# Performance work log

Measured on AMD Instinct MI355X. Metric: run time of the kernel, lower is better.

## Reference

```python
import jax, jax.numpy as jnp
import numpy as np

H = 16   # multiheads
DH = 64  # head_dim


def setup_inputs() -> dict:
    key = jax.random.key(0)
    ks = jax.random.split(key, 9)
    B, S, D = 4, 2048, H * DH
    scale = 1.0 / np.sqrt(D)
    return {
        "Q_seq": jax.random.normal(ks[0], (B, S, D), dtype=jnp.float32),
        "K_seq": jax.random.normal(ks[1], (B, S, D), dtype=jnp.float32),
        "V_seq": jax.random.normal(ks[2], (B, S, D), dtype=jnp.float32),
        "WQ_w": jax.random.normal(ks[3], (D, D), dtype=jnp.float32) * scale,
        "WQ_b": jax.random.normal(ks[4], (D,), dtype=jnp.float32) * 0.02,
        "WK_w": jax.random.normal(ks[5], (D, D), dtype=jnp.float32) * scale,
        "WK_b": jax.random.normal(ks[6], (D,), dtype=jnp.float32) * 0.02,
        "WV_w": jax.random.normal(ks[7], (D, D), dtype=jnp.float32) * scale,
        "WV_b": jax.random.normal(ks[8], (D,), dtype=jnp.float32) * 0.02,
    }


def reference(Q_seq, K_seq, V_seq, WQ_w, WQ_b, WK_w, WK_b, WV_w, WV_b):
    B, Sq, D = Q_seq.shape
    Sk = K_seq.shape[1]
    # torch nn.Linear: y = x @ W.T + b
    Q = (Q_seq @ WQ_w.T + WQ_b).reshape(B, Sq, H, DH).transpose(0, 2, 1, 3)  # bhqd
    K = (K_seq @ WK_w.T + WK_b).reshape(B, Sk, H, DH).transpose(0, 2, 1, 3)  # bhkd
    V = (V_seq @ WV_w.T + WV_b).reshape(B, Sk, H, DH).transpose(0, 2, 1, 3)  # bhkd
    inv_sqrt_d = jnp.float32(1.0 / np.sqrt(DH))
    A = jnp.einsum('bhqd,bhkd->bhqk', Q, K) * inv_sqrt_d
    A = jax.nn.softmax(A, axis=-1)
    O = jnp.einsum('bhqk,bhkd->bhqd', A, V)
    return O.transpose(0, 2, 1, 3).reshape(B, Sq, H * DH)
```

## Files before the change

### kernel.cpp

```cpp
#include <hip/hip_runtime.h>

#define HH 16
#define DHH 64
#define BB 4
#define SS 2048
#define DD 1024

typedef __attribute__((ext_vector_type(8))) short short8;
typedef __attribute__((ext_vector_type(4))) float f32x4;
typedef __attribute__((ext_vector_type(16))) float f32x16;

__device__ __forceinline__ unsigned short f2bf(float f) {
  union { float f; unsigned int u; } v; v.f = f;
  unsigned int r = v.u + 0x7fffu + ((v.u >> 16) & 1u);
  return (unsigned short)(r >> 16);
}
__device__ __forceinline__ unsigned cvt_pk_bf16(float a, float b) {
  unsigned r;
  asm("v_cvt_pk_bf16_f32 %0, %1, %2" : "=v"(r) : "v"(a), "v"(b));
  return r;
}

__global__ __launch_bounds__(256) void proj_kernel(
    const float* __restrict__ X, const float* __restrict__ W,
    const float* __restrict__ bias, unsigned short* __restrict__ out,
    int mode, float scale)
{
  __shared__ unsigned short As[128 * 40];
  __shared__ unsigned short Bs[128 * 40];

  const int t    = threadIdx.x;
  const int pb   = blockIdx.x;
  const int lb   = (pb & 7) * 64 + (pb >> 3);
  const int m0   = (lb >> 3) * 128;
  const int n0   = (lb & 7) * 128;
  const int rowA = t >> 3;
  const int kc   = (t & 7) * 4;
  const int lane = t & 63;
  const int wid  = t >> 6;
  const int wm   = (wid >> 1) * 64;
  const int wn   = (wid & 1) * 64;
  const int g    = lane >> 4;
  const int c    = lane & 15;

  f32x4 acc[4][4];
#pragma unroll
  for (int i = 0; i < 4; ++i)
#pragma unroll
    for (int j = 0; j < 4; ++j) acc[i][j] = (f32x4){0.f, 0.f, 0.f, 0.f};

  float4 xa[4], wb[4];
#pragma unroll
  for (int p4 = 0; p4 < 4; ++p4) {
    const int r = p4 * 32 + rowA;
    xa[p4] = *reinterpret_cast<const float4*>(X + (size_t)(m0 + r) * DD + kc);
    wb[p4] = *reinterpret_cast<const float4*>(W + (size_t)(n0 + r) * DD + kc);
  }

  for (int kt = 0; kt < 32; ++kt) {
    __syncthreads();
#pragma unroll
    for (int p4 = 0; p4 < 4; ++p4) {
      const int r = p4 * 32 + rowA;
      unsigned* da = reinterpret_cast<unsigned*>(&As[r * 40 + kc]);
      unsigned* db = reinterpret_cast<unsigned*>(&Bs[r * 40 + kc]);
      da[0] = cvt_pk_bf16(xa[p4].x, xa[p4].y);
      da[1] = cvt_pk_bf16(xa[p4].z, xa[p4].w);
      db[0] = cvt_pk_bf16(wb[p4].x, wb[p4].y);
      db[1] = cvt_pk_bf16(wb[p4].z, wb[p4].w);
    }
    __syncthreads();
    if (kt < 31) {
#pragma unroll
      for (int p4 = 0; p4 < 4; ++p4) {
        const int r = p4 * 32 + rowA;
        xa[p4] = *reinterpret_cast<const float4*>(
            X + (size_t)(m0 + r) * DD + (kt + 1) * 32 + kc);
        wb[p4] = *reinterpret_cast<const float4*>(
            W + (size_t)(n0 + r) * DD + (kt + 1) * 32 + kc);
      }
    }
    short8 a[4], b[4];
#pragma unroll
    for (int mf = 0; mf < 4; ++mf)
      a[mf] = *reinterpret_cast<const short8*>(&As[(wm + mf * 16 + c) * 40 + g * 8]);
#pragma unroll
    for (int nf = 0; nf < 4; ++nf)
      b[nf] = *reinterpret_cast<const short8*>(&Bs[(wn + nf * 16 + c) * 40 + g * 8]);
#pragma unroll
    for (int mf = 0; mf < 4; ++mf)
#pragma unroll
      for (int nf = 0; nf < 4; ++nf)
        acc[mf][nf] = __builtin_amdgcn_mfma_f32_16x16x32_bf16(
            a[mf], b[nf], acc[mf][nf], 0, 0, 0);
  }

#pragma unroll
  for (int nf = 0; nf < 4; ++nf) {
    const int col  = n0 + wn + nf * 16 + c;
    const float bv = bias[col];
    const int hcol = col >> 6;
    const int dcol = col & 63;
#pragma unroll
    for (int mf = 0; mf < 4; ++mf) {
      const int row0 = m0 + wm + mf * 16 + g * 4;
      const int bi   = row0 >> 11;
      const int s0   = row0 & 2047;
      if (mode < 2) {
        const size_t base = ((size_t)(bi * HH + hcol) * SS + s0) * DHH + dcol;
#pragma unroll
        for (int r = 0; r < 4; ++r)
          out[base + (size_t)r * DHH] = f2bf((acc[mf][nf][r] + bv) * scale);
      } else {
        const size_t base = ((size_t)(bi * HH + hcol) * DHH + dcol) * SS + s0;
        unsigned* dp = reinterpret_cast<unsigned*>(out + base);
        dp[0] = cvt_pk_bf16(acc[mf][nf][0] + bv, acc[mf][nf][1] + bv);
        dp[1] = cvt_pk_bf16(acc[mf][nf][2] + bv, acc[mf][nf][3] + bv);
      }
    }
  }
}

__global__ __launch_bounds__(256, 4) void attn_kernel(
    const unsigned short* __restrict__ Qb,
    const unsigned short* __restrict__ Kb,
    const unsigned short* __restrict__ Vt,
    float* __restrict__ O)
{
  __shared__ unsigned short sm[16384];

  const int t    = threadIdx.x;
  const int lane = t & 63;
  const int w    = t >> 6;
  const int h    = lane >> 5;
  const int c5   = lane & 31;
  const int cx   = c5 & 7;

  const int p  = blockIdx.x;
  const int l  = (p & 7) * 128 + (p >> 3);
  const int bh = l >> 4;
  const int qb = l & 15;
  const int q0 = qb * 128 + w * 32;

  const unsigned short* Qp = Qb + (size_t)bh * SS * DHH;
  const unsigned short* Kp = Kb + (size_t)bh * SS * DHH;
  const unsigned short* Vp = Vt + (size_t)bh * DHH * SS;

  const int srow   = t >> 3;
  const int schunk = (t & 7) ^ (srow & 7);

  auto STAGE = [&](int buf, int kt) {
    const int kk0 = kt * 64;
#pragma unroll
    for (int j = 0; j < 2; ++j) {
      const unsigned short* gk = Kp + (size_t)(kk0 + j * 32 + srow) * DHH + schunk * 8;
      const unsigned short* gv = Vp + (size_t)(j * 32 + srow) * SS + kk0 + schunk * 8;
      __builtin_amdgcn_global_load_lds(
          (const __attribute__((address_space(1))) void*)gk,
          (__attribute__((address_space(3))) void*)(sm + buf * 8192 + j * 2048 + w * 512),
          16, 0, 0);
      __builtin_amdgcn_global_load_lds(
          (const __attribute__((address_space(1))) void*)gv,
          (__attribute__((address_space(3))) void*)(sm + buf * 8192 + 4096 + j * 2048 + w * 512),
          16, 0, 0);
    }
  };

  short8 bq[4];
#pragma unroll
  for (int k4 = 0; k4 < 4; ++k4)
    bq[k4] = *reinterpret_cast<const short8*>(
        Qp + (size_t)(q0 + c5) * DHH + k4 * 16 + h * 8);

  STAGE(0, 0);

  f32x16 oa0, oa1;
#pragma unroll
  for (int i = 0; i < 16; ++i) { oa0[i] = 0.f; oa1[i] = 0.f; }
  float m_run = -1e30f, l_part = 0.f;

  __syncthreads();

  for (int kt = 0; kt < SS / 64; ++kt) {
    const int buf = kt & 1;
    if (kt + 1 < SS / 64) STAGE(buf ^ 1, kt + 1);

    const unsigned short* Kl = sm + buf * 8192;
    const unsigned short* Vl = Kl + 4096;

    f32x16 st0, st1;
#pragma unroll
    for (int i = 0; i < 16; ++i) { st0[i] = 0.f; st1[i] = 0.f; }
#pragma unroll
    for (int k4 = 0; k4 < 4; ++k4) {
      const int pos = ((2 * k4 + h) ^ cx) * 8;
      short8 ak0 = *reinterpret_cast<const short8*>(Kl + c5 * 64 + pos);
      short8 ak1 = *reinterpret_cast<const short8*>(Kl + (32 + c5) * 64 + pos);
      st0 = __builtin_amdgcn_mfma_f32_32x32x16_bf16(ak0, bq[k4], st0, 0, 0, 0);
      st1 = __builtin_amdgcn_mfma_f32_32x32x16_bf16(ak1, bq[k4], st1, 0, 0, 0);
    }

    float mloc = st0[0];
#pragma unroll
    for (int i = 1; i < 16; ++i) mloc = fmaxf(mloc, st0[i]);
#pragma unroll
    for (int i = 0; i < 16; ++i) mloc = fmaxf(mloc, st1[i]);
    mloc = fmaxf(mloc, __shfl_xor(mloc, 32));

    if (!__all(mloc <= m_run + 11.0f)) {
      const float mn = fmaxf(m_run, mloc);
      const float al = exp2f(m_run - mn);
      l_part *= al;
#pragma unroll
      for (int i = 0; i < 16; ++i) { oa0[i] *= al; oa1[i] *= al; }
      m_run = mn;
    }

#pragma unroll
    for (int i = 0; i < 16; ++i) { st0[i] = exp2f(st0[i] - m_run); l_part += st0[i]; }
#pragma unroll
    for (int i = 0; i < 16; ++i) { st1[i] = exp2f(st1[i] - m_run); l_part += st1[i]; }

    unsigned pw[16];
#pragma unroll
    for (int m4 = 0; m4 < 4; ++m4)
#pragma unroll
      for (int t2 = 0; t2 < 2; ++t2) {
        pw[m4 * 2 + t2]     = cvt_pk_bf16(st0[m4 * 4 + 2 * t2], st0[m4 * 4 + 2 * t2 + 1]);
        pw[8 + m4 * 2 + t2] = cvt_pk_bf16(st1[m4 * 4 + 2 * t2], st1[m4 * 4 + 2 * t2 + 1]);
      }

#pragma unroll
    for (int ks = 0; ks < 4; ++ks) {
      union { unsigned u[4]; short8 s8; } pbu;
#pragma unroll
      for (int t2 = 0; t2 < 2; ++t2) {
        const unsigned e  = pw[4 * ks + t2];
        const unsigned o  = pw[4 * ks + 2 + t2];
        const unsigned ce = (unsigned)__shfl_xor((int)e, 32);
        const unsigned co = (unsigned)__shfl_xor((int)o, 32);
        pbu.u[t2]     = h ? co : e;
        pbu.u[2 + t2] = h ? o  : ce;
      }
      const int vpos = ((2 * ks + h) ^ cx) * 8;
      short8 av0 = *reinterpret_cast<const short8*>(Vl + c5 * 64 + vpos);
      short8 av1 = *reinterpret_cast<const short8*>(Vl + (32 + c5) * 64 + vpos);
      oa0 = __builtin_amdgcn_mfma_f32_32x32x16_bf16(av0, pbu.s8, oa0, 0, 0, 0);
      oa1 = __builtin_amdgcn_mfma_f32_32x32x16_bf16(av1, pbu.s8, oa1, 0, 0, 0);
    }
    __syncthreads();
  }

  const float lt  = l_part + __shfl_xor(l_part, 32);
  const float inv = 1.f / lt;
  const int b = bh >> 4, hd = bh & 15;
  float* Orow = O + ((size_t)(b * SS) + q0 + c5) * DD + hd * DHH;
#pragma unroll
  for (int m4 = 0; m4 < 4; ++m4) {
    f32x4 v0, v1;
#pragma unroll
    for (int r = 0; r < 4; ++r) {
      v0[r] = oa0[m4 * 4 + r] * inv;
      v1[r] = oa1[m4 * 4 + r] * inv;
    }
    *reinterpret_cast<f32x4*>(Orow + m4 * 8 + 4 * h)      = v0;
    *reinterpret_cast<f32x4*>(Orow + 32 + m4 * 8 + 4 * h) = v1;
  }
}

extern "C" void kernel_launch(void* const* d_in, const int* in_sizes, int n_in,
                              void* d_out, int out_size, void* d_ws, size_t ws_size,
                              hipStream_t stream) {
  (void)in_sizes; (void)n_in; (void)out_size; (void)ws_size;
  const float* Xq = (const float*)d_in[0];
  const float* Xk = (const float*)d_in[1];
  const float* Xv = (const float*)d_in[2];
  const float* WQ = (const float*)d_in[3];
  const float* bQ = (const float*)d_in[4];
  const float* WK = (const float*)d_in[5];
  const float* bK = (const float*)d_in[6];
  const float* WV = (const float*)d_in[7];
  const float* bV = (const float*)d_in[8];
  float* O = (float*)d_out;

  const size_t elems = (size_t)BB * HH * SS * DHH;
  unsigned short* Qbuf = (unsigned short*)d_ws;
  unsigned short* Kbuf = Qbuf + elems;
  unsigned short* Vbuf = Kbuf + elems;

  const float CLOG = 0.125f * 1.4426950408889634f;
  proj_kernel<<<512, 256, 0, stream>>>(Xq, WQ, bQ, Qbuf, 0, CLOG);
  proj_kernel<<<512, 256, 0, stream>>>(Xk, WK, bK, Kbuf, 1, 1.0f);
  proj_kernel<<<512, 256, 0, stream>>>(Xv, WV, bV, Vbuf, 2, 1.0f);

  attn_kernel<<<1024, 256, 0, stream>>>(Qbuf, Kbuf, Vbuf, O);
}
```

Before: 380.3 us.

## Pre-convert inputs to bf16 and restructure projection and attention inner loops

Adds a separate fp32-to-bf16 conversion pass so the projection GEMM can stream bf16 tiles into swizzled, double-buffered LDS with global_load_lds, using a larger K step. The attention kernel folds the running max into the accumulator init, uses max3 reductions, raw v_exp_f32, permlane32 swaps instead of shuffles, and s_setprio around MFMA blocks. This removes in-loop conversion and register staging from the GEMM and trims VALU work in softmax, at the cost of extra kernel launches and a full read/write pass over the activations and weights.

```diff
diff --git a/kernel.cpp b/kernel.cpp
--- a/kernel.cpp
+++ b/kernel.cpp
@@ -5,6 +5,8 @@
 #define BB 4
 #define SS 2048
 #define DD 1024
+#define XN 8388608
+#define WN 1048576
 
 typedef __attribute__((ext_vector_type(8))) short short8;
 typedef __attribute__((ext_vector_type(4))) float f32x4;
@@ -20,28 +22,75 @@
   asm("v_cvt_pk_bf16_f32 %0, %1, %2" : "=v"(r) : "v"(a), "v"(b));
   return r;
 }
+__device__ __forceinline__ float fast_exp2(float x) {
+  float r;
+  asm("v_exp_f32 %0, %1" : "=v"(r) : "v"(x));
+  return r;
+}
+__device__ __forceinline__ float m3(float a, float b, float c) {
+  float r;
+  asm("v_max3_f32 %0, %1, %2, %3" : "=v"(r) : "v"(a), "v"(b), "v"(c));
+  return r;
+}
+__device__ __forceinline__ void plswap(unsigned& a, unsigned& b) {
+  auto r = __builtin_amdgcn_permlane32_swap(a, b, false, false);
+  a = r[0]; b = r[1];
+}
+
+__global__ __launch_bounds__(256) void conv_kernel(
+    const float* __restrict__ X, const float* __restrict__ W,
+    unsigned short* __restrict__ Xb, unsigned short* __restrict__ Wb)
+{
+  const size_t gid = (size_t)blockIdx.x * 256 + threadIdx.x;
+  const float* src; unsigned short* dst; size_t off;
+  if (gid < XN / 8) { src = X; dst = Xb; off = gid * 8; }
+  else              { src = W; dst = Wb; off = (gid - XN / 8) * 8; }
+  const float4 a = *reinterpret_cast<const float4*>(src + off);
+  const float4 b = *reinterpret_cast<const float4*>(src + off + 4);
+  unsigned r[4] = { cvt_pk_bf16(a.x, a.y), cvt_pk_bf16(a.z, a.w),
+                    cvt_pk_bf16(b.x, b.y), cvt_pk_bf16(b.z, b.w) };
+  *reinterpret_cast<uint4*>(dst + off) = *reinterpret_cast<uint4*>(r);
+}
 
 __global__ __launch_bounds__(256) void proj_kernel(
-    const float* __restrict__ X, const float* __restrict__ W,
+    const unsigned short* __restrict__ Xb, const unsigned short* __restrict__ Wb,
     const float* __restrict__ bias, unsigned short* __restrict__ out,
     int mode, float scale)
 {
-  __shared__ unsigned short As[128 * 40];
-  __shared__ unsigned short Bs[128 * 40];
+  __shared__ unsigned short As[2][128 * 64];
+  __shared__ unsigned short Bs[2][128 * 64];
 
   const int t    = threadIdx.x;
   const int pb   = blockIdx.x;
   const int lb   = (pb & 7) * 64 + (pb >> 3);
   const int m0   = (lb >> 3) * 128;
   const int n0   = (lb & 7) * 128;
-  const int rowA = t >> 3;
-  const int kc   = (t & 7) * 4;
   const int lane = t & 63;
   const int wid  = t >> 6;
   const int wm   = (wid >> 1) * 64;
   const int wn   = (wid & 1) * 64;
   const int g    = lane >> 4;
   const int c    = lane & 15;
+  const int cx   = c & 7;
+
+  const int srow = t >> 3;
+  const int sch  = (t & 7) ^ (srow & 7);
+
+  auto STAGE = [&](int buf, int k0) {
+#pragma unroll
+    for (int i = 0; i < 4; ++i) {
+      const unsigned short* ga = Xb + (size_t)(m0 + i * 32 + srow) * DD + k0 + sch * 8;
+      const unsigned short* gb = Wb + (size_t)(n0 + i * 32 + srow) * DD + k0 + sch * 8;
+      __builtin_amdgcn_global_load_lds(
+          (const __attribute__((address_space(1))) void*)ga,
+          (__attribute__((address_space(3))) void*)(&As[buf][0] + i * 2048 + wid * 512),
+          16, 0, 0);
+      __builtin_amdgcn_global_load_lds(
+          (const __attribute__((address_space(1))) void*)gb,
+          (__attribute__((address_space(3))) void*)(&Bs[buf][0] + i * 2048 + wid * 512),
+          16, 0, 0);
+    }
+  };
 
   f32x4 acc[4][4];
 #pragma unroll
@@ -49,50 +98,38 @@
 #pragma unroll
     for (int j = 0; j < 4; ++j) acc[i][j] = (f32x4){0.f, 0.f, 0.f, 0.f};
 
-  float4 xa[4], wb[4];
-#pragma unroll
-  for (int p4 = 0; p4 < 4; ++p4) {
-    const int r = p4 * 32 + rowA;
-    xa[p4] = *reinterpret_cast<const float4*>(X + (size_t)(m0 + r) * DD + kc);
-    wb[p4] = *reinterpret_cast<const float4*>(W + (size_t)(n0 + r) * DD + kc);
-  }
-
-  for (int kt = 0; kt < 32; ++kt) {
+  STAGE(0, 0);
+
+  for (int kt = 0; kt < 16; ++kt) {
+    const int buf = kt & 1;
     __syncthreads();
-#pragma unroll
-    for (int p4 = 0; p4 < 4; ++p4) {
-      const int r = p4 * 32 + rowA;
-      unsigned* da = reinterpret_cast<unsigned*>(&As[r * 40 + kc]);
-      unsigned* db = reinterpret_cast<unsigned*>(&Bs[r * 40 + kc]);
-      da[0] = cvt_pk_bf16(xa[p4].x, xa[p4].y);
-      da[1] = cvt_pk_bf16(xa[p4].z, xa[p4].w);
-      db[0] = cvt_pk_bf16(wb[p4].x, wb[p4].y);
-      db[1] = cvt_pk_bf16(wb[p4].z, wb[p4].w);
-    }
-    __syncthreads();
-    if (kt < 31) {
-#pragma unroll
-      for (int p4 = 0; p4 < 4; ++p4) {
-        const int r = p4 * 32 + rowA;
-        xa[p4] = *reinterpret_cast<const float4*>(
-            X + (size_t)(m0 + r) * DD + (kt + 1) * 32 + kc);
-        wb[p4] = *reinterpret_cast<const float4*>(
-            W + (size_t)(n0 + r) * DD + (kt + 1) * 32 + kc);
-      }
-    }
-    short8 a[4], b[4];
-#pragma unroll
-    for (int mf = 0; mf < 4; ++mf)
-      a[mf] = *reinterpret_cast<const short8*>(&As[(wm + mf * 16 + c) * 40 + g * 8]);
-#pragma unroll
-    for (int nf = 0; nf < 4; ++nf)
-      b[nf] = *reinterpret_cast<const short8*>(&Bs[(wn + nf * 16 + c) * 40 + g * 8]);
-#pragma unroll
-    for (int mf = 0; mf < 4; ++mf)
-#pragma unroll
-      for (int nf = 0; nf < 4; ++nf)
-        acc[mf][nf] = __builtin_amdgcn_mfma_f32_16x16x32_bf16(
-            a[mf], b[nf], acc[mf][nf], 0, 0, 0);
+    if (kt < 15) STAGE(buf ^ 1, (kt + 1) * 64);
+
+    short8 a[4][2], b[4][2];
+#pragma unroll
+    for (int mf = 0; mf < 4; ++mf) {
+      const int row = wm + mf * 16 + c;
+#pragma unroll
+      for (int ks = 0; ks < 2; ++ks)
+        a[mf][ks] = *reinterpret_cast<const short8*>(
+            &As[buf][row * 64 + (((ks * 4 + g) ^ cx)) * 8]);
+    }
+#pragma unroll
+    for (int nf = 0; nf < 4; ++nf) {
+      const int row = wn + nf * 16 + c;
+#pragma unroll
+      for (int ks = 0; ks < 2; ++ks)
+        b[nf][ks] = *reinterpret_cast<const short8*>(
+            &Bs[buf][row * 64 + (((ks * 4 + g) ^ cx)) * 8]);
+    }
+#pragma unroll
+    for (int ks = 0; ks < 2; ++ks)
+#pragma unroll
+      for (int mf = 0; mf < 4; ++mf)
+#pragma unroll
+        for (int nf = 0; nf < 4; ++nf)
+          acc[mf][nf] = __builtin_amdgcn_mfma_f32_16x16x32_bf16(
+              a[mf][ks], b[nf][ks], acc[mf][nf], 0, 0, 0);
   }
 
 #pragma unroll
@@ -177,7 +214,7 @@
   f32x16 oa0, oa1;
 #pragma unroll
   for (int i = 0; i < 16; ++i) { oa0[i] = 0.f; oa1[i] = 0.f; }
-  float m_run = -1e30f, l_part = 0.f;
+  float m_run = 0.f, l_part = 0.f;
 
   __syncthreads();
 
@@ -189,8 +226,11 @@
     const unsigned short* Vl = Kl + 4096;
 
     f32x16 st0, st1;
-#pragma unroll
-    for (int i = 0; i < 16; ++i) { st0[i] = 0.f; st1[i] = 0.f; }
+    const float nm = -m_run;
+#pragma unroll
+    for (int i = 0; i < 16; ++i) { st0[i] = nm; st1[i] = nm; }
+
+    __builtin_amdgcn_s_setprio(1);
 #pragma unroll
     for (int k4 = 0; k4 < 4; ++k4) {
       const int pos = ((2 * k4 + h) ^ cx) * 8;
@@ -199,27 +239,54 @@
       st0 = __builtin_amdgcn_mfma_f32_32x32x16_bf16(ak0, bq[k4], st0, 0, 0, 0);
       st1 = __builtin_amdgcn_mfma_f32_32x32x16_bf16(ak1, bq[k4], st1, 0, 0, 0);
     }
-
-    float mloc = st0[0];
-#pragma unroll
-    for (int i = 1; i < 16; ++i) mloc = fmaxf(mloc, st0[i]);
-#pragma unroll
-    for (int i = 0; i < 16; ++i) mloc = fmaxf(mloc, st1[i]);
-    mloc = fmaxf(mloc, __shfl_xor(mloc, 32));
-
-    if (!__all(mloc <= m_run + 11.0f)) {
-      const float mn = fmaxf(m_run, mloc);
-      const float al = exp2f(m_run - mn);
+    __builtin_amdgcn_s_setprio(0);
+
+    float a0 = m3(st0[0], st0[1], st0[2]);
+    float a1 = m3(st0[3], st0[4], st0[5]);
+    float a2 = m3(st0[6], st0[7], st0[8]);
+    float a3 = m3(st0[9], st0[10], st0[11]);
+    float a4 = m3(st0[12], st0[13], st0[14]);
+    float a5 = m3(st0[15], st1[0], st1[1]);
+    float a6 = m3(st1[2], st1[3], st1[4]);
+    float a7 = m3(st1[5], st1[6], st1[7]);
+    float a8 = m3(st1[8], st1[9], st1[10]);
+    float a9 = m3(st1[11], st1[12], st1[13]);
+    float a10 = fmaxf(st1[14], st1[15]);
+    float b0 = m3(a0, a1, a2);
+    float b1 = m3(a3, a4, a5);
+    float b2 = m3(a6, a7, a8);
+    float b3 = m3(a9, a10, b0);
+    float mloc = m3(b1, b2, b3);
+    {
+      unsigned ua = __float_as_uint(mloc), ub = ua;
+      plswap(ua, ub);
+      mloc = fmaxf(__uint_as_float(ua), __uint_as_float(ub));
+    }
+
+    if (!__all(mloc <= 11.0f)) {
+      const float d  = fmaxf(mloc, 0.f);
+      const float al = exp2f(-d);
       l_part *= al;
 #pragma unroll
       for (int i = 0; i < 16; ++i) { oa0[i] *= al; oa1[i] *= al; }
-      m_run = mn;
-    }
-
-#pragma unroll
-    for (int i = 0; i < 16; ++i) { st0[i] = exp2f(st0[i] - m_run); l_part += st0[i]; }
-#pragma unroll
-    for (int i = 0; i < 16; ++i) { st1[i] = exp2f(st1[i] - m_run); l_part += st1[i]; }
+#pragma unroll
+      for (int i = 0; i < 16; ++i) { st0[i] -= d; st1[i] -= d; }
+      m_run += d;
+    }
+
+    float l0 = 0.f, l1 = 0.f, l2 = 0.f, l3 = 0.f;
+#pragma unroll
+    for (int i = 0; i < 16; i += 4) {
+      st0[i]     = fast_exp2(st0[i]);     l0 += st0[i];
+      st0[i + 1] = fast_exp2(st0[i + 1]); l1 += st0[i + 1];
+      st0[i + 2] = fast_exp2(st0[i + 2]); l2 += st0[i + 2];
+      st0[i + 3] = fast_exp2(st0[i + 3]); l3 += st0[i + 3];
+      st1[i]     = fast_exp2(st1[i]);     l0 += st1[i];
+      st1[i + 1] = fast_exp2(st1[i + 1]); l1 += st1[i + 1];
+      st1[i + 2] = fast_exp2(st1[i + 2]); l2 += st1[i + 2];
+      st1[i + 3] = fast_exp2(st1[i + 3]); l3 += st1[i + 3];
+    }
+    l_part += (l0 + l1) + (l2 + l3);
 
     unsigned pw[16];
 #pragma unroll
@@ -230,17 +297,17 @@
         pw[8 + m4 * 2 + t2] = cvt_pk_bf16(st1[m4 * 4 + 2 * t2], st1[m4 * 4 + 2 * t2 + 1]);
       }
 
+    __builtin_amdgcn_s_setprio(1);
 #pragma unroll
     for (int ks = 0; ks < 4; ++ks) {
       union { unsigned u[4]; short8 s8; } pbu;
 #pragma unroll
       for (int t2 = 0; t2 < 2; ++t2) {
-        const unsigned e  = pw[4 * ks + t2];
-        const unsigned o  = pw[4 * ks + 2 + t2];
-        const unsigned ce = (unsigned)__shfl_xor((int)e, 32);
-        const unsigned co = (unsigned)__shfl_xor((int)o, 32);
-        pbu.u[t2]     = h ? co : e;
-        pbu.u[2 + t2] = h ? o  : ce;
+        unsigned a = pw[4 * ks + t2];
+        unsigned b = pw[4 * ks + 2 + t2];
+        plswap(a, b);
+        pbu.u[t2]     = a;
+        pbu.u[2 + t2] = b;
       }
       const int vpos = ((2 * ks + h) ^ cx) * 8;
       short8 av0 = *reinterpret_cast<const short8*>(Vl + c5 * 64 + vpos);
@@ -248,10 +315,13 @@
       oa0 = __builtin_amdgcn_mfma_f32_32x32x16_bf16(av0, pbu.s8, oa0, 0, 0, 0);
       oa1 = __builtin_amdgcn_mfma_f32_32x32x16_bf16(av1, pbu.s8, oa1, 0, 0, 0);
     }
+    __builtin_amdgcn_s_setprio(0);
     __syncthreads();
   }
 
-  const float lt  = l_part + __shfl_xor(l_part, 32);
+  unsigned la = __float_as_uint(l_part), lb = la;
+  plswap(la, lb);
+  const float lt  = __uint_as_float(la) + __uint_as_float(lb);
   const float inv = 1.f / lt;
   const int b = bh >> 4, hd = bh & 15;
   float* Orow = O + ((size_t)(b * SS) + q0 + c5) * DD + hd * DHH;
@@ -287,11 +357,18 @@
   unsigned short* Qbuf = (unsigned short*)d_ws;
   unsigned short* Kbuf = Qbuf + elems;
   unsigned short* Vbuf = Kbuf + elems;
+  unsigned short* Xc   = Vbuf + elems;
+  unsigned short* Wc   = Xc + (size_t)XN;
 
   const float CLOG = 0.125f * 1.4426950408889634f;
-  proj_kernel<<<512, 256, 0, stream>>>(Xq, WQ, bQ, Qbuf, 0, CLOG);
-  proj_kernel<<<512, 256, 0, stream>>>(Xk, WK, bK, Kbuf, 1, 1.0f);
-  proj_kernel<<<512, 256, 0, stream>>>(Xv, WV, bV, Vbuf, 2, 1.0f);
+  const int cgrid = (XN + WN) / 8 / 256;
+
+  conv_kernel<<<cgrid, 256, 0, stream>>>(Xq, WQ, Xc, Wc);
+  proj_kernel<<<512, 256, 0, stream>>>(Xc, Wc, bQ, Qbuf, 0, CLOG);
+  conv_kernel<<<cgrid, 256, 0, stream>>>(Xk, WK, Xc, Wc);
+  proj_kernel<<<512, 256, 0, stream>>>(Xc, Wc, bK, Kbuf, 1, 1.0f);
+  conv_kernel<<<cgrid, 256, 0, stream>>>(Xv, WV, Xc, Wc);
+  proj_kernel<<<512, 256, 0, stream>>>(Xc, Wc, bV, Vbuf, 2, 1.0f);
 
   attn_kernel<<<1024, 256, 0, stream>>>(Qbuf, Kbuf, Vbuf, O);
 }
```

Result: faster. 324.3 us (-14.7%).
